# Kernel optimization log

Hardware: AMD Instinct MI355X
Metric: run time of the kernel (lower is better)

## Reference

```python
import jax, jax.numpy as jnp
import numpy as np

EPS = 1e-8

def _conv(x, w, b=None):
    # NCHW conv, stride 1, SAME padding (k=3, pad=1)
    y = jax.lax.conv_general_dilated(x, w, (1, 1), 'SAME',
                                     dimension_numbers=('NCHW', 'OIHW', 'NCHW'))
    if b is not None:
        y = y + b[None, :, None, None]
    return y

def setup_inputs() -> dict:
    key = jax.random.key(0)
    ks = jax.random.split(key, 6)
    B, C, H, W = 512, 1024, 8, 8
    return {
        'x': jax.random.normal(ks[0], (B, C, H, W), jnp.float32),
        'w1_1': jax.random.normal(ks[1], (1, 1, 3, 3), jnp.float32) * 0.1,
        'w5': jax.random.normal(ks[2], (4, 2, 3, 3), jnp.float32) * 0.1,
        'b5': jax.random.normal(ks[3], (4,), jnp.float32) * 0.1,
        'w6': jax.random.normal(ks[4], (1, 4, 3, 3), jnp.float32) * 0.1,
        'b6': jax.random.normal(ks[5], (1,), jnp.float32) * 0.1,
    }

def reference(x, w1_1, w5, b5, w6, b6):
    B, C, H, W = x.shape  # H == W == 8 by module construction
    m = jnp.max(x, axis=1, keepdims=True)  # [B,1,H,W] channel max
    # 2x2 non-overlapping windows, torch unfold layout -> [B,1,(H/2)*(W/2),4]
    win = m.reshape(B, 1, H // 2, 2, W // 2, 2)
    win = win.transpose(0, 1, 2, 4, 3, 5).reshape(B, 1, (H // 2) * (W // 2), 4)
    # probabilistic pooling: clean inf/nan/negatives, sample per window
    winc = jnp.where(jnp.isinf(win) | jnp.isnan(win) | (win < 0), EPS, win)
    skey = jax.random.key(1)
    idx = jax.random.categorical(skey, winc, axis=-1)  # softmax(winc) multinomial
    mo2 = jnp.take_along_axis(winc, idx[..., None], axis=-1)[..., 0]
    mo2 = mo2.reshape(B, 1, H // 2, W // 2)
    # adaptive max/avg pool (4,4) on 8x8 == 2x2 pooling, reuse windows
    mo3 = win.max(axis=-1).reshape(B, 1, H // 2, W // 2)
    ao4 = win.mean(axis=-1).reshape(B, 1, H // 2, W // 2)
    out2 = 0.1 * mo2 + 0.6 * mo3 + 0.3 * ao4
    out2 = _conv(out2, w1_1)  # bias-free 1->1 conv
    out2 = jax.image.resize(out2, (B, 1, H, W), method='bilinear')  # align_corners=False
    out1 = jnp.concatenate([m, out2], axis=1)  # [B,2,H,W]
    gate = jax.nn.sigmoid(_conv(jax.nn.relu(_conv(out1, w5, b5)), w6, b6))  # [B,1,H,W]
    return jax.nn.relu(x * gate)
```

## Files before the change

### kernel.cpp

```cpp
#include <hip/hip_runtime.h>
#include <math.h>

#define C_DIM 1024
#define HW 64
#define NTHREADS 512
#define C_PER 32

#define EPSV 1e-8f
#define TINYF 1.17549435e-38f

#define THREEFRY_PARTITIONABLE 1

__device__ __forceinline__ void threefry2x32_01(unsigned x0, unsigned x1,
                                                unsigned& o0, unsigned& o1) {
    const unsigned ks0 = 0u, ks1 = 1u, ks2 = 0x1BD11BDBu;
    x0 += ks0; x1 += ks1;
#define TF_R(r) { x0 += x1; x1 = (x1 << (r)) | (x1 >> (32 - (r))); x1 ^= x0; }
    TF_R(13) TF_R(15) TF_R(26) TF_R(6)
    x0 += ks1; x1 += ks2 + 1u;
    TF_R(17) TF_R(29) TF_R(16) TF_R(24)
    x0 += ks2; x1 += ks0 + 2u;
    TF_R(13) TF_R(15) TF_R(26) TF_R(6)
    x0 += ks0; x1 += ks1 + 3u;
    TF_R(17) TF_R(29) TF_R(16) TF_R(24)
    x0 += ks1; x1 += ks2 + 4u;
    TF_R(13) TF_R(15) TF_R(26) TF_R(6)
    x0 += ks2; x1 += ks0 + 5u;
#undef TF_R
    o0 = x0; o1 = x1;
}

__device__ __forceinline__ unsigned jax_random_bits(unsigned n) {
#if THREEFRY_PARTITIONABLE
    unsigned o0, o1;
    threefry2x32_01(0u, n, o0, o1);
    return o0 ^ o1;
#else
    unsigned o0, o1;
    if (n < 16384u) { threefry2x32_01(n, n + 16384u, o0, o1); return o0; }
    else            { threefry2x32_01(n - 16384u, n, o0, o1); return o1; }
#endif
}

__device__ __forceinline__ bool bad_val(float v) {
    return ((__float_as_uint(v) & 0x7F800000u) == 0x7F800000u) || (v < 0.0f);
}

__global__ __launch_bounds__(NTHREADS) void sa_fused_kernel(
    const float* __restrict__ x,
    const float* __restrict__ w11,
    const float* __restrict__ w5,
    const float* __restrict__ b5,
    const float* __restrict__ w6,
    const float* __restrict__ b6,
    float* __restrict__ out)
{
    const int b = blockIdx.x;
    const int t = threadIdx.x;
    const int hw4 = t & 15;
    const int cs  = t >> 4;

    const float4* __restrict__ xb = (const float4*)x + (size_t)b * (C_DIM * HW / 4);
    float4* __restrict__ ob = (float4*)out + (size_t)b * (C_DIM * HW / 4);

    __shared__ float4 red[NTHREADS];
    __shared__ float sm[64];
    __shared__ float sg[64];
    __shared__ float sa16[16];
    __shared__ float sb16[16];
    __shared__ float so2[64];
    __shared__ float shid[4 * 64];
    __shared__ float sgate[64];

    float4 pm = make_float4(-INFINITY, -INFINITY, -INFINITY, -INFINITY);
    const int c0 = cs * C_PER;
#pragma unroll 8
    for (int i = 0; i < C_PER; ++i) {
        float4 v = xb[(c0 + i) * 16 + hw4];
        pm.x = fmaxf(pm.x, v.x); pm.y = fmaxf(pm.y, v.y);
        pm.z = fmaxf(pm.z, v.z); pm.w = fmaxf(pm.w, v.w);
    }
    red[t] = pm;
    __syncthreads();
#pragma unroll
    for (int s = 16; s >= 1; s >>= 1) {
        if (cs < s) {
            float4 a = red[t];
            float4 o = red[t + s * 16];
            a.x = fmaxf(a.x, o.x); a.y = fmaxf(a.y, o.y);
            a.z = fmaxf(a.z, o.z); a.w = fmaxf(a.w, o.w);
            red[t] = a;
        }
        __syncthreads();
    }
    if (t < 16) {
        float4 a = red[t];
        sm[t * 4 + 0] = a.x; sm[t * 4 + 1] = a.y;
        sm[t * 4 + 2] = a.z; sm[t * 4 + 3] = a.w;
    }
    if (t < 64) {
        unsigned n = (unsigned)(b * 64 + t);
        unsigned bits = jax_random_bits(n);
        float f = __uint_as_float(0x3F800000u | (bits >> 9)) - 1.0f;
        float u = f + TINYF;
        u = fmaxf(TINYF, u);
        sg[t] = -logf(-logf(u));
    }
    __syncthreads();

    if (t < 16) {
        int h2 = t >> 2, w2 = t & 3;
        float win[4], winc[4];
#pragma unroll
        for (int j = 0; j < 4; ++j) {
            int hh = 2 * h2 + (j >> 1), ww = 2 * w2 + (j & 1);
            float v = sm[hh * 8 + ww];
            win[j] = v;
            winc[j] = bad_val(v) ? EPSV : v;
        }
        int idx = 0;
        float best = winc[0] + sg[t * 4 + 0];
#pragma unroll
        for (int j = 1; j < 4; ++j) {
            float s = winc[j] + sg[t * 4 + j];
            if (s > best) { best = s; idx = j; }
        }
        float mo2 = winc[idx];
        float mo3 = fmaxf(fmaxf(win[0], win[1]), fmaxf(win[2], win[3]));
        float ssum = ((win[0] + win[1]) + win[2]) + win[3];
        float ao4 = ssum * 0.25f;
        sa16[t] = 0.1f * mo2 + 0.6f * mo3 + 0.3f * ao4;
    }
    __syncthreads();

    if (t < 16) {
        int i = t >> 2, j = t & 3;
        float acc = 0.0f;
#pragma unroll
        for (int dy = -1; dy <= 1; ++dy) {
            int yy = i + dy;
            if (yy < 0 || yy > 3) continue;
#pragma unroll
            for (int dx = -1; dx <= 1; ++dx) {
                int xx = j + dx;
                if (xx < 0 || xx > 3) continue;
                acc += sa16[yy * 4 + xx] * w11[(dy + 1) * 3 + (dx + 1)];
            }
        }
        sb16[t] = acc;
    }
    __syncthreads();

    if (t < 64) {
        int y = t >> 3, xx2 = t & 7;
        float sy = (y + 0.5f) * 0.5f - 0.5f;
        float sx = (xx2 + 0.5f) * 0.5f - 0.5f;
        float fy = fminf(fmaxf(sy, 0.0f), 3.0f);
        float fx = fminf(fmaxf(sx, 0.0f), 3.0f);
        int iy0 = (int)floorf(fy); int iy1 = min(iy0 + 1, 3); float ry = fy - (float)iy0;
        int ix0 = (int)floorf(fx); int ix1 = min(ix0 + 1, 3); float rx = fx - (float)ix0;
        float v00 = sb16[iy0 * 4 + ix0], v01 = sb16[iy0 * 4 + ix1];
        float v10 = sb16[iy1 * 4 + ix0], v11 = sb16[iy1 * 4 + ix1];
        float top = v00 * (1.0f - rx) + v01 * rx;
        float bot = v10 * (1.0f - rx) + v11 * rx;
        so2[t] = top * (1.0f - ry) + bot * ry;
    }
    __syncthreads();

    if (t < 64) {
        int y = t >> 3, x2 = t & 7;
        float a0 = b5[0], a1 = b5[1], a2 = b5[2], a3 = b5[3];
#pragma unroll
        for (int dy = -1; dy <= 1; ++dy) {
            int yy = y + dy;
            if (yy < 0 || yy > 7) continue;
#pragma unroll
            for (int dx = -1; dx <= 1; ++dx) {
                int xx = x2 + dx;
                if (xx < 0 || xx > 7) continue;
                float i0 = sm[yy * 8 + xx];
                float i1 = so2[yy * 8 + xx];
                int kk = (dy + 1) * 3 + (dx + 1);
                a0 += i0 * w5[0 * 18 + kk] + i1 * w5[0 * 18 + 9 + kk];
                a1 += i0 * w5[1 * 18 + kk] + i1 * w5[1 * 18 + 9 + kk];
                a2 += i0 * w5[2 * 18 + kk] + i1 * w5[2 * 18 + 9 + kk];
                a3 += i0 * w5[3 * 18 + kk] + i1 * w5[3 * 18 + 9 + kk];
            }
        }
        shid[0 * 64 + t] = fmaxf(a0, 0.0f);
        shid[1 * 64 + t] = fmaxf(a1, 0.0f);
        shid[2 * 64 + t] = fmaxf(a2, 0.0f);
        shid[3 * 64 + t] = fmaxf(a3, 0.0f);
    }
    __syncthreads();

    if (t < 64) {
        int y = t >> 3, x2 = t & 7;
        float acc = b6[0];
#pragma unroll
        for (int dy = -1; dy <= 1; ++dy) {
            int yy = y + dy;
            if (yy < 0 || yy > 7) continue;
#pragma unroll
            for (int dx = -1; dx <= 1; ++dx) {
                int xx = x2 + dx;
                if (xx < 0 || xx > 7) continue;
                int kk = (dy + 1) * 3 + (dx + 1);
                int p = yy * 8 + xx;
                acc += shid[0 * 64 + p] * w6[0 + kk]
                     + shid[1 * 64 + p] * w6[9 + kk]
                     + shid[2 * 64 + p] * w6[18 + kk]
                     + shid[3 * 64 + p] * w6[27 + kk];
            }
        }
        sgate[t] = 1.0f / (1.0f + expf(-acc));
    }
    __syncthreads();

    float4 g4;
    g4.x = sgate[hw4 * 4 + 0]; g4.y = sgate[hw4 * 4 + 1];
    g4.z = sgate[hw4 * 4 + 2]; g4.w = sgate[hw4 * 4 + 3];
#pragma unroll 8
    for (int i = 0; i < C_PER; ++i) {
        float4 v = xb[(c0 + i) * 16 + hw4];
        float4 o;
        o.x = fmaxf(v.x * g4.x, 0.0f);
        o.y = fmaxf(v.y * g4.y, 0.0f);
        o.z = fmaxf(v.z * g4.z, 0.0f);
        o.w = fmaxf(v.w * g4.w, 0.0f);
        ob[(c0 + i) * 16 + hw4] = o;
    }
}

extern "C" void kernel_launch(void* const* d_in, const int* in_sizes, int n_in,
                              void* d_out, int out_size, void* d_ws, size_t ws_size,
                              hipStream_t stream) {
    const float* x   = (const float*)d_in[0];
    const float* w11 = (const float*)d_in[1];
    const float* w5  = (const float*)d_in[2];
    const float* b5  = (const float*)d_in[3];
    const float* w6  = (const float*)d_in[4];
    const float* b6  = (const float*)d_in[5];
    float* out = (float*)d_out;

    int B = in_sizes[0] / (C_DIM * HW);
    sa_fused_kernel<<<dim3(B), dim3(NTHREADS), 0, stream>>>(x, w11, w5, b5, w6, b6, out);
}
```

Before: 266.2 us.

## Split fused kernel into gate-computation and gate-apply kernels with wave-level reduction

Splits the single per-batch kernel into two. The first computes the gate map: it reads x with fully coalesced contiguous float4 loads, reduces with wave shuffles plus a small shared-memory step, and runs the serial gate stages inside one wavefront using wave barriers instead of block barriers. The second applies the gate over four times as many blocks, which raises parallelism for the streaming pass. In exchange it adds a second launch and a round trip through a workspace buffer, and x is still read twice but now across kernel boundaries, so the second read may be less likely to hit in cache.

```diff
diff --git a/kernel.cpp b/kernel.cpp
--- a/kernel.cpp
+++ b/kernel.cpp
@@ -3,13 +3,11 @@
 
 #define C_DIM 1024
 #define HW 64
-#define NTHREADS 512
-#define C_PER 32
-
+#define NT_A 512
+#define NT_B 256
+#define F4_PER_BATCH 16384
 #define EPSV 1e-8f
 #define TINYF 1.17549435e-38f
-
-#define THREEFRY_PARTITIONABLE 1
 
 __device__ __forceinline__ void threefry2x32_01(unsigned x0, unsigned x1,
                                                 unsigned& o0, unsigned& o1) {
@@ -31,98 +29,88 @@
 }
 
 __device__ __forceinline__ unsigned jax_random_bits(unsigned n) {
-#if THREEFRY_PARTITIONABLE
     unsigned o0, o1;
     threefry2x32_01(0u, n, o0, o1);
     return o0 ^ o1;
-#else
-    unsigned o0, o1;
-    if (n < 16384u) { threefry2x32_01(n, n + 16384u, o0, o1); return o0; }
-    else            { threefry2x32_01(n - 16384u, n, o0, o1); return o1; }
-#endif
 }
 
 __device__ __forceinline__ bool bad_val(float v) {
     return ((__float_as_uint(v) & 0x7F800000u) == 0x7F800000u) || (v < 0.0f);
 }
 
-__global__ __launch_bounds__(NTHREADS) void sa_fused_kernel(
+__global__ __launch_bounds__(NT_A) void sa_gate_kernel(
     const float* __restrict__ x,
     const float* __restrict__ w11,
     const float* __restrict__ w5,
     const float* __restrict__ b5,
     const float* __restrict__ w6,
     const float* __restrict__ b6,
-    float* __restrict__ out)
+    float* __restrict__ gate_out)
 {
     const int b = blockIdx.x;
     const int t = threadIdx.x;
-    const int hw4 = t & 15;
-    const int cs  = t >> 4;
-
-    const float4* __restrict__ xb = (const float4*)x + (size_t)b * (C_DIM * HW / 4);
-    float4* __restrict__ ob = (float4*)out + (size_t)b * (C_DIM * HW / 4);
-
-    __shared__ float4 red[NTHREADS];
+
+    const float4* __restrict__ xb = (const float4*)x + (size_t)b * F4_PER_BATCH;
+
+    __shared__ float4 red[8 * 16];
     __shared__ float sm[64];
-    __shared__ float sg[64];
     __shared__ float sa16[16];
     __shared__ float sb16[16];
     __shared__ float so2[64];
     __shared__ float shid[4 * 64];
-    __shared__ float sgate[64];
 
     float4 pm = make_float4(-INFINITY, -INFINITY, -INFINITY, -INFINITY);
-    const int c0 = cs * C_PER;
-#pragma unroll 8
-    for (int i = 0; i < C_PER; ++i) {
-        float4 v = xb[(c0 + i) * 16 + hw4];
+#pragma unroll 16
+    for (int i = 0; i < 32; ++i) {
+        float4 v = xb[t + NT_A * i];
         pm.x = fmaxf(pm.x, v.x); pm.y = fmaxf(pm.y, v.y);
         pm.z = fmaxf(pm.z, v.z); pm.w = fmaxf(pm.w, v.w);
     }
-    red[t] = pm;
+#pragma unroll
+    for (int off = 16; off <= 32; off <<= 1) {
+        pm.x = fmaxf(pm.x, __shfl_xor(pm.x, off, 64));
+        pm.y = fmaxf(pm.y, __shfl_xor(pm.y, off, 64));
+        pm.z = fmaxf(pm.z, __shfl_xor(pm.z, off, 64));
+        pm.w = fmaxf(pm.w, __shfl_xor(pm.w, off, 64));
+    }
+    const int wv = t >> 6, lane = t & 63;
+    if (lane < 16) red[wv * 16 + lane] = pm;
     __syncthreads();
-#pragma unroll
-    for (int s = 16; s >= 1; s >>= 1) {
-        if (cs < s) {
-            float4 a = red[t];
-            float4 o = red[t + s * 16];
+    if (t >= 64) return;
+
+    if (t < 16) {
+        float4 a = red[t];
+#pragma unroll
+        for (int w = 1; w < 8; ++w) {
+            float4 o = red[w * 16 + t];
             a.x = fmaxf(a.x, o.x); a.y = fmaxf(a.y, o.y);
             a.z = fmaxf(a.z, o.z); a.w = fmaxf(a.w, o.w);
-            red[t] = a;
-        }
-        __syncthreads();
-    }
-    if (t < 16) {
-        float4 a = red[t];
+        }
         sm[t * 4 + 0] = a.x; sm[t * 4 + 1] = a.y;
         sm[t * 4 + 2] = a.z; sm[t * 4 + 3] = a.w;
     }
-    if (t < 64) {
-        unsigned n = (unsigned)(b * 64 + t);
-        unsigned bits = jax_random_bits(n);
-        float f = __uint_as_float(0x3F800000u | (bits >> 9)) - 1.0f;
-        float u = f + TINYF;
-        u = fmaxf(TINYF, u);
-        sg[t] = -logf(-logf(u));
-    }
-    __syncthreads();
+    __builtin_amdgcn_wave_barrier();
 
     if (t < 16) {
         int h2 = t >> 2, w2 = t & 3;
-        float win[4], winc[4];
+        float win[4], winc[4], sg[4];
 #pragma unroll
         for (int j = 0; j < 4; ++j) {
             int hh = 2 * h2 + (j >> 1), ww = 2 * w2 + (j & 1);
             float v = sm[hh * 8 + ww];
             win[j] = v;
             winc[j] = bad_val(v) ? EPSV : v;
+            unsigned n = (unsigned)(b * 64 + t * 4 + j);
+            unsigned bits = jax_random_bits(n);
+            float f = __uint_as_float(0x3F800000u | (bits >> 9)) - 1.0f;
+            float u = fmaxf(TINYF, f + TINYF);
+            sg[j] = -logf(-logf(u));
         }
         int idx = 0;
-        float best = winc[0] + sg[t * 4 + 0];
+        float best = winc[0] + sg[0];
 #pragma unroll
         for (int j = 1; j < 4; ++j) {
-            float s = winc[j] + sg[t * 4 + j];
+            float s = winc[j] + sg[j];
             if (s > best) { best = s; idx = j; }
         }
         float mo2 = winc[idx];
@@ -131,7 +119,7 @@
         float ao4 = ssum * 0.25f;
         sa16[t] = 0.1f * mo2 + 0.6f * mo3 + 0.3f * ao4;
     }
-    __syncthreads();
+    __builtin_amdgcn_wave_barrier();
 
     if (t < 16) {
         int i = t >> 2, j = t & 3;
@@ -149,9 +137,9 @@
         }
         sb16[t] = acc;
     }
-    __syncthreads();
-
-    if (t < 64) {
+    __builtin_amdgcn_wave_barrier();
+
+    {
         int y = t >> 3, xx2 = t & 7;
         float sy = (y + 0.5f) * 0.5f - 0.5f;
         float sx = (xx2 + 0.5f) * 0.5f - 0.5f;
@@ -165,9 +153,9 @@
         float bot = v10 * (1.0f - rx) + v11 * rx;
         so2[t] = top * (1.0f - ry) + bot * ry;
     }
-    __syncthreads();
-
-    if (t < 64) {
+    __builtin_amdgcn_wave_barrier();
+
+    {
         int y = t >> 3, x2 = t & 7;
         float a0 = b5[0], a1 = b5[1], a2 = b5[2], a3 = b5[3];
 #pragma unroll
@@ -192,9 +180,9 @@
         shid[2 * 64 + t] = fmaxf(a2, 0.0f);
         shid[3 * 64 + t] = fmaxf(a3, 0.0f);
     }
-    __syncthreads();
-
-    if (t < 64) {
+    __builtin_amdgcn_wave_barrier();
+
+    {
         int y = t >> 3, x2 = t & 7;
         float acc = b6[0];
 #pragma unroll
@@ -213,22 +201,35 @@
                      + shid[3 * 64 + p] * w6[27 + kk];
             }
         }
-        sgate[t] = 1.0f / (1.0f + expf(-acc));
-    }
-    __syncthreads();
-
-    float4 g4;
-    g4.x = sgate[hw4 * 4 + 0]; g4.y = sgate[hw4 * 4 + 1];
-    g4.z = sgate[hw4 * 4 + 2]; g4.w = sgate[hw4 * 4 + 3];
+        gate_out[b * 64 + t] = 1.0f / (1.0f + expf(-acc));
+    }
+}
+
+__global__ __launch_bounds__(NT_B) void sa_apply_kernel(
+    const float* __restrict__ x,
+    const float* __restrict__ gate,
+    float* __restrict__ out)
+{
+    const int bid = blockIdx.x;
+    const int t = threadIdx.x;
+    const int b = bid >> 2;
+    const size_t base = (size_t)bid * 4096;
+
+    const float4* __restrict__ x4 = (const float4*)x;
+    float4* __restrict__ o4 = (float4*)out;
+
+    const float4 gv = ((const float4*)(gate + b * 64))[t & 15];
+
 #pragma unroll 8
-    for (int i = 0; i < C_PER; ++i) {
-        float4 v = xb[(c0 + i) * 16 + hw4];
+    for (int i = 0; i < 16; ++i) {
+        size_t idx = base + t + NT_B * i;
+        float4 v = x4[idx];
         float4 o;
-        o.x = fmaxf(v.x * g4.x, 0.0f);
-        o.y = fmaxf(v.y * g4.y, 0.0f);
-        o.z = fmaxf(v.z * g4.z, 0.0f);
-        o.w = fmaxf(v.w * g4.w, 0.0f);
-        ob[(c0 + i) * 16 + hw4] = o;
+        o.x = fmaxf(v.x * gv.x, 0.0f);
+        o.y = fmaxf(v.y * gv.y, 0.0f);
+        o.z = fmaxf(v.z * gv.z, 0.0f);
+        o.w = fmaxf(v.w * gv.w, 0.0f);
+        o4[idx] = o;
     }
 }
 
@@ -241,8 +242,10 @@
     const float* b5  = (const float*)d_in[3];
     const float* w6  = (const float*)d_in[4];
     const float* b6  = (const float*)d_in[5];
-    float* out = (float*)d_out;
+    float* out  = (float*)d_out;
+    float* gate = (float*)d_ws;
 
     int B = in_sizes[0] / (C_DIM * HW);
-    sa_fused_kernel<<<dim3(B), dim3(NTHREADS), 0, stream>>>(x, w11, w5, b5, w6, b6, out);
-}
+    sa_gate_kernel<<<dim3(B), dim3(NT_A), 0, stream>>>(x, w11, w5, b5, w6, b6, gate);
+    sa_apply_kernel<<<dim3(B * 4), dim3(NT_B), 0, stream>>>(x, gate, out);
+}
```

Measured after the change: 259.8 us. 2.4% less time.
